# Optimization experiments

Measured on AMD Instinct MI355X. Metric: run time of the kernel, lower is better.

Reference implementation:

```python
import jax, jax.numpy as jnp
import numpy as np

B, S, WIDTH, M = 2, 240, 128, 20
PAD = 16


def setup_inputs() -> dict:
    key = jax.random.key(0)
    ks = jax.random.split(key, 10)
    scale = 1.0 / (WIDTH * WIDTH)
    inp = {
        "x": jax.random.normal(ks[0], (B, S, S, 3), jnp.float32),
        "fc0_w": jax.random.normal(ks[1], (5, WIDTH), jnp.float32) * 0.1,
        "fc0_b": jnp.zeros((WIDTH,), jnp.float32),
        # 5 spectral layers, complex weights stored as [..., 2] = (real, imag)
        "spec_w1": jax.random.uniform(ks[2], (5, WIDTH, WIDTH, M, M, 2), jnp.float32) * scale,
        "spec_w2": jax.random.uniform(ks[3], (5, WIDTH, WIDTH, M, M, 2), jnp.float32) * scale,
        # 5 residual 1x1 convs
        "w_w": jax.random.normal(ks[4], (5, WIDTH, WIDTH), jnp.float32) / np.sqrt(WIDTH),
        "w_b": jnp.zeros((5, WIDTH), jnp.float32),
        "fc1_w": jax.random.normal(ks[5], (WIDTH, WIDTH), jnp.float32) / np.sqrt(WIDTH),
        "fc1_b": jnp.zeros((WIDTH,), jnp.float32),
        # 4 heads (u, v, p, T): width->64->1
        "head1_w": jax.random.normal(ks[6], (4, WIDTH, 64), jnp.float32) / np.sqrt(WIDTH),
        "head1_b": jnp.zeros((4, 64), jnp.float32),
        "head2_w": jax.random.normal(ks[7], (4, 64, 1), jnp.float32) / 8.0,
        "head2_b": jnp.zeros((4, 1), jnp.float32),
    }
    return inp


def _spectral_conv(h, w1, w2):
    # h: (B, C, H, W) real; w1, w2: (C_in, C_out, M, M) complex64
    Hh, Ww = h.shape[-2], h.shape[-1]
    ft = jnp.fft.rfft2(h)  # (B, C, H, W//2+1)
    o1 = jnp.einsum('bixy,ioxy->boxy', ft[:, :, :M, :M], w1)
    o2 = jnp.einsum('bixy,ioxy->boxy', ft[:, :, -M:, :M], w2)
    out_ft = jnp.zeros((h.shape[0], w1.shape[1], Hh, Ww // 2 + 1), jnp.complex64)
    out_ft = out_ft.at[:, :, :M, :M].set(o1).at[:, :, -M:, :M].set(o2)
    return jnp.fft.irfft2(out_ft, s=(Hh, Ww))


def reference(x, fc0_w, fc0_b, spec_w1, spec_w2, w_w, w_b, fc1_w, fc1_b,
              head1_w, head1_b, head2_w, head2_b):
    Bn, sx, sy = x.shape[0], x.shape[1], x.shape[2]
    gx = jnp.broadcast_to(jnp.linspace(0.0, 1.0, sx, dtype=x.dtype)[None, :, None, None], (Bn, sx, sy, 1))
    gy = jnp.broadcast_to(jnp.linspace(0.0, 1.0, sy, dtype=x.dtype)[None, None, :, None], (Bn, sx, sy, 1))
    x1 = jnp.concatenate([x, gx, gy], axis=-1)          # (B, S, S, 5)
    h = x1 @ fc0_w + fc0_b                              # lift -> (B, S, S, width)
    h = jnp.transpose(h, (0, 3, 1, 2))                  # (B, width, S, S)
    h = jnp.pad(h, ((0, 0), (0, 0), (0, PAD), (0, PAD)))
    c1 = spec_w1[..., 0] + 1j * spec_w1[..., 1]
    c2 = spec_w2[..., 0] + 1j * spec_w2[..., 1]
    for i in range(5):
        s = _spectral_conv(h, c1[i], c2[i])
        lin = jnp.einsum('bchw,oc->bohw', h, w_w[i]) + w_b[i][None, :, None, None]
        h = s + lin
        if i < 4:
            h = jax.nn.gelu(h, approximate=False)
    h = h[..., :-PAD, :-PAD]
    h = jnp.transpose(h, (0, 2, 3, 1))                  # (B, S, S, width)
    h = jax.nn.gelu(h @ fc1_w + fc1_b, approximate=False)
    h1 = jax.nn.gelu(jnp.einsum('bhwc,kcd->kbhwd', h, head1_w)
                     + head1_b[:, None, None, None, :], approximate=False)
    out = jnp.einsum('kbhwd,kdo->kbhwo', h1, head2_w) + head2_b[:, None, None, None, :]
    return (out[0], out[1], out[2], out[3])  # u, v, p, T each (B, S, S, 1)
```

## Files before the change

### kernel.cpp

```cpp
#include <hip/hip_runtime.h>
#include <math.h>


#define SZ_H   (2ull*256*256*128)
#define O_HA   0ull
#define O_HB   (O_HA + SZ_H)
#define O_G    (O_HB + SZ_H)
#define SZ_G   (2ull*256*20*128*2)
#define O_FTT  (O_G + SZ_G)
#define SZ_FT  (2ull*40*20*128*2)
#define O_OFT  (O_FTT + SZ_FT)
#define O_EY   (O_OFT + SZ_FT)
#define SZ_EY  (256ull*20*2)
#define O_EX   (O_EY + SZ_EY)
#define SZ_EX  (256ull*40*2)
#define O_EXI  (O_EX + SZ_EX)
#define O_WWT  (O_EXI + SZ_EX)
#define SZ_WWT 81920ull
#define O_PART (O_WWT + SZ_WWT)
#define SZ_PART (8ull*204800*2)

static __device__ __forceinline__ float gelu_f(float v) {
    return 0.5f * v * (1.0f + erff(v * 0.70710678118654752f));
}

__global__ void k_prep(const float* __restrict__ w_w, float* __restrict__ ws) {
    int i = blockIdx.x * 256 + threadIdx.x;
    const float STEP = 6.2831853071795864769f / 256.0f;
    if (i < 5120) {
        int ky = i % 20, y = i / 20;
        int t = (ky * y) & 255;
        float th = t * STEP;
        ws[O_EY + 2*(size_t)i]     = cosf(th);
        ws[O_EY + 2*(size_t)i + 1] = -sinf(th);
    } else if (i < 15360) {
        int m = i - 5120; int j = m % 40, x = m / 40;
        int kx = (j < 20) ? j : (216 + j);
        int t = (kx * x) & 255;
        float th = t * STEP;
        ws[O_EX + 2*(size_t)m]     = cosf(th);
        ws[O_EX + 2*(size_t)m + 1] = -sinf(th);
    } else if (i < 25600) {
        int m = i - 15360; int j = m % 40, x = m / 40;
        int kx = (j < 20) ? j : (216 + j);
        int t = (kx * x) & 255;
        float th = t * STEP;
        ws[O_EXI + 2*(size_t)m]     = cosf(th);
        ws[O_EXI + 2*(size_t)m + 1] = sinf(th);
    } else {
        int m = i - 25600;
        if (m < 81920) {
            int l = m >> 14, r = m & 16383;
            int ic = r >> 7, oc = r & 127;
            ws[O_WWT + m] = w_w[(size_t)l*16384 + oc*128 + ic];
        }
    }
}

__global__ __launch_bounds__(256) void k_fc0(const float* __restrict__ xin,
        const float* __restrict__ w, const float* __restrict__ bv,
        float4* __restrict__ H4) {
    size_t e = (size_t)blockIdx.x * 256 + threadIdx.x;
    int c4 = (int)(e & 31) * 4;
    int y = (int)((e >> 5) & 255);
    int x = (int)((e >> 13) & 255);
    int b = (int)(e >> 21);
    float4 h = make_float4(0.f, 0.f, 0.f, 0.f);
    if (x < 240 && y < 240) {
        const float* xp = xin + (((size_t)(b*240 + x))*240 + y)*3;
        float x0 = xp[0], x1 = xp[1], x2 = xp[2];
        float gx = x*(1.0f/239.0f), gy = y*(1.0f/239.0f);
        float4 w0 = *(const float4*)&w[c4];
        float4 w1 = *(const float4*)&w[128 + c4];
        float4 w2 = *(const float4*)&w[256 + c4];
        float4 w3 = *(const float4*)&w[384 + c4];
        float4 w4 = *(const float4*)&w[512 + c4];
        float4 bb = *(const float4*)&bv[c4];
        h.x = bb.x + x0*w0.x + x1*w1.x + x2*w2.x + gx*w3.x + gy*w4.x;
        h.y = bb.y + x0*w0.y + x1*w1.y + x2*w2.y + gx*w3.y + gy*w4.y;
        h.z = bb.z + x0*w0.z + x1*w1.z + x2*w2.z + gx*w3.z + gy*w4.z;
        h.w = bb.w + x0*w0.w + x1*w1.w + x2*w2.w + gx*w3.w + gy*w4.w;
    }
    H4[e] = h;
}

__global__ __launch_bounds__(256) void k_ydft(const float* __restrict__ H,
        const float* __restrict__ Ey, float2* __restrict__ G) {
    int b = blockIdx.x >> 8, x = blockIdx.x & 255;
    int c = threadIdx.x & 127;
    int yq = __builtin_amdgcn_readfirstlane((int)(threadIdx.x >> 7));
    const float* Hrow = H + ((size_t)(b*256 + x)) * 256 * 128;
    float ar[20], ai[20];
    #pragma unroll
    for (int k = 0; k < 20; k++) { ar[k] = 0.f; ai[k] = 0.f; }
    for (int i = 0; i < 128; i++) {
        int y = yq*128 + i;
        float v = Hrow[(size_t)y*128 + c];
        const float* e = Ey + (size_t)y*40;
        #pragma unroll
        for (int k = 0; k < 20; k++) {
            ar[k] = fmaf(v, e[2*k],   ar[k]);
            ai[k] = fmaf(v, e[2*k+1], ai[k]);
        }
    }
    __shared__ float red[20][128][2];
    if (yq == 1) {
        #pragma unroll
        for (int k = 0; k < 20; k++) { red[k][c][0] = ar[k]; red[k][c][1] = ai[k]; }
    }
    __syncthreads();
    if (yq == 0) {
        float2* Gp = G + ((size_t)(b*256 + x))*20*128;
        #pragma unroll
        for (int k = 0; k < 20; k++)
            Gp[k*128 + c] = make_float2(ar[k] + red[k][c][0], ai[k] + red[k][c][1]);
    }
}

__global__ __launch_bounds__(256) void k_xdft(const float2* __restrict__ G,
        const float* __restrict__ Ex, float2* __restrict__ ftT) {
    int t = blockIdx.x;
    int ch = t & 3, jq = (t >> 2) & 3, ky = (t >> 4) % 20, b = t / 320;
    int cl = threadIdx.x & 31;
    int xq = threadIdx.x >> 5;
    int c = ch*32 + cl;
    int j0 = jq*10;
    float ar[10], ai[10];
    #pragma unroll
    for (int k = 0; k < 10; k++) { ar[k] = 0.f; ai[k] = 0.f; }
    for (int i = 0; i < 32; i++) {
        int x = xq*32 + i;
        float2 g = G[(((size_t)(b*256 + x))*20 + ky)*128 + c];
        const float2* e2 = (const float2*)(Ex + (size_t)x*80) + j0;
        #pragma unroll
        for (int k = 0; k < 10; k++) {
            float2 e = e2[k];
            ar[k] = fmaf(g.x, e.x, fmaf(-g.y, e.y, ar[k]));
            ai[k] = fmaf(g.x, e.y, fmaf( g.y, e.x, ai[k]));
        }
    }
    #pragma unroll
    for (int k = 0; k < 10; k++) {
        ar[k] += __shfl_xor(ar[k], 32);
        ai[k] += __shfl_xor(ai[k], 32);
    }
    __shared__ float red[3][10][32][2];
    int wid = threadIdx.x >> 6;
    int sub = threadIdx.x & 63;
    if (wid > 0 && sub < 32) {
        #pragma unroll
        for (int k = 0; k < 10; k++) { red[wid-1][k][cl][0] = ar[k]; red[wid-1][k][cl][1] = ai[k]; }
    }
    __syncthreads();
    if (wid == 0 && sub < 32) {
        #pragma unroll
        for (int k = 0; k < 10; k++) {
            float rr = ar[k], ii = ai[k];
            #pragma unroll
            for (int q = 0; q < 3; q++) { rr += red[q][k][cl][0]; ii += red[q][k][cl][1]; }
            ftT[((size_t)c*2 + b)*800 + (size_t)(j0 + k)*20 + ky] = make_float2(rr, ii);
        }
    }
}

__global__ __launch_bounds__(448) void k_modemix(const float2* __restrict__ w1,
        const float2* __restrict__ w2, const float2* __restrict__ ftT,
        float2* __restrict__ outp, int ic_per) {
    int bid = blockIdx.x & 255;
    int icq = blockIdx.x >> 8;
    int oc = bid >> 1;
    int mh = bid & 1;
    int tid = threadIdx.x;
    if (tid >= 400) return;
    int wsel = tid / 200;
    int m = mh*200 + (tid % 200);
    int jk = wsel*400 + m;
    const float2* wb = wsel ? w2 : w1;
    int ic0 = icq * ic_per;
    float ar0=0.f, ai0=0.f, ar1=0.f, ai1=0.f;
    #pragma unroll 4
    for (int i = 0; i < ic_per; i++) {
        int ic = ic0 + i;
        float2 wv = wb[((size_t)(ic*128 + oc))*400 + m];
        float2 f0 = ftT[(size_t)ic*1600 + jk];
        float2 f1 = ftT[(size_t)ic*1600 + 800 + jk];
        ar0 = fmaf(f0.x, wv.x, fmaf(-f0.y, wv.y, ar0));
        ai0 = fmaf(f0.x, wv.y, fmaf( f0.y, wv.x, ai0));
        ar1 = fmaf(f1.x, wv.x, fmaf(-f1.y, wv.y, ar1));
        ai1 = fmaf(f1.x, wv.y, fmaf( f1.y, wv.x, ai1));
    }
    float2* o = outp + (size_t)icq * 204800;
    o[(size_t)jk*128 + oc]         = make_float2(ar0, ai0);
    o[(size_t)(800 + jk)*128 + oc] = make_float2(ar1, ai1);
}

__global__ __launch_bounds__(512) void k_modered(const float2* __restrict__ part,
        float2* __restrict__ oft) {
    int i = blockIdx.x * 512 + threadIdx.x;
    if (i >= 204800) return;
    float2 s = part[i];
    #pragma unroll
    for (int q = 1; q < 8; q++) {
        float2 p = part[(size_t)q*204800 + i];
        s.x += p.x; s.y += p.y;
    }
    oft[i] = s;
}

__global__ __launch_bounds__(256) void k_xidft(const float2* __restrict__ oft,
        const float* __restrict__ Exi, float2* __restrict__ T) {
    int b = blockIdx.x >> 7, xq = blockIdx.x & 127;
    int oc = threadIdx.x & 127;
    int xs = __builtin_amdgcn_readfirstlane((int)(threadIdx.x >> 7));
    int x = xq*2 + xs;
    float ar[20], ai[20];
    #pragma unroll
    for (int k = 0; k < 20; k++) { ar[k] = 0.f; ai[k] = 0.f; }
    const float2* ob = oft + (size_t)b*800*128;
    for (int j = 0; j < 40; j++) {
        float er = Exi[(size_t)x*80 + 2*j], ei = Exi[(size_t)x*80 + 2*j + 1];
        #pragma unroll
        for (int k = 0; k < 20; k++) {
            float2 o = ob[(size_t)(j*20 + k)*128 + oc];
            ar[k] = fmaf(o.x, er, fmaf(-o.y, ei, ar[k]));
            ai[k] = fmaf(o.x, ei, fmaf( o.y, er, ai[k]));
        }
    }
    float2* Tp = T + ((size_t)(b*256 + x))*20*128;
    #pragma unroll
    for (int k = 0; k < 20; k++) Tp[k*128 + oc] = make_float2(ar[k], ai[k]);
}

__global__ __launch_bounds__(256) void k_spec_lin(const float* __restrict__ H,
        const float2* __restrict__ T, const float* __restrict__ wwT,
        const float* __restrict__ wb, float* __restrict__ Hout, int do_gelu) {
    int yg = blockIdx.x & 3;
    int x  = (blockIdx.x >> 2) & 255;
    int b  = blockIdx.x >> 10;
    int tid = threadIdx.x;
    int lane = tid & 63;
    int wv = __builtin_amdgcn_readfirstlane(tid >> 6);
    int oc0 = wv * 32;
    int y0 = yg * 64;
    __shared__ float hl[64][129];
    const float* Hbase = H + (((size_t)(b*256 + x))*256 + y0)*128;
    #pragma unroll
    for (int it = 0; it < 8; it++) {
        int i = tid + it*256;
        int pi = i >> 5, c4 = (i & 31)*4;
        float4 v = *(const float4*)&Hbase[(size_t)pi*128 + c4];
        hl[pi][c4] = v.x; hl[pi][c4+1] = v.y; hl[pi][c4+2] = v.z; hl[pi][c4+3] = v.w;
    }
    float csr[20], csi[20];
    {
        int y = y0 + lane;
        #pragma unroll
        for (int k = 0; k < 20; k++) {
            int t = (k * y) & 255;
            float th = t * (6.2831853071795864769f/256.0f);
            float f = (k == 0 ? 1.0f : 2.0f) * (1.0f/65536.0f);
            csr[k] = f * __cosf(th);
            csi[k] = f * __sinf(th);
        }
    }
    __syncthreads();
    float acc[32];
    #pragma unroll
    for (int o = 0; o < 32; o++) acc[o] = 0.f;
    for (int ic = 0; ic < 128; ic++) {
        float t = hl[lane][ic];
        const float* wr = &wwT[(size_t)ic*128 + oc0];
        #pragma unroll
        for (int o4 = 0; o4 < 8; o4++) {
            float4 w = *(const float4*)&wr[o4*4];
            acc[o4*4]   = fmaf(t, w.x, acc[o4*4]);
            acc[o4*4+1] = fmaf(t, w.y, acc[o4*4+1]);
            acc[o4*4+2] = fmaf(t, w.z, acc[o4*4+2]);
            acc[o4*4+3] = fmaf(t, w.w, acc[o4*4+3]);
        }
    }
    const float2* Tp = T + ((size_t)(b*256 + x))*20*128 + oc0;
    for (int k = 0; k < 20; k++) {
        const float2* tr = Tp + (size_t)k*128;
        float cr = csr[k], ci = csi[k];
        #pragma unroll
        for (int o = 0; o < 32; o++) {
            float2 tv = tr[o];
            acc[o] = fmaf(tv.x, cr, fmaf(-tv.y, ci, acc[o]));
        }
    }
    __syncthreads();
    const float* bp = &wb[oc0];
    #pragma unroll
    for (int o = 0; o < 32; o++) {
        float v = acc[o] + bp[o];
        if (do_gelu) v = gelu_f(v);
        hl[lane][oc0 + o] = v;
    }
    __syncthreads();
    float* Obase = Hout + (((size_t)(b*256 + x))*256 + y0)*128;
    #pragma unroll
    for (int it = 0; it < 32; it++) {
        int i = tid + it*256;
        int pi = i >> 7, c = i & 127;
        Obase[(size_t)pi*128 + c] = hl[pi][c];
    }
}

__global__ __launch_bounds__(512) void k_tail(const float* __restrict__ H,
        const float* __restrict__ fc1_w, const float* __restrict__ fc1_b,
        const float* __restrict__ h1w, const float* __restrict__ h1b,
        const float* __restrict__ h2w, const float* __restrict__ h2b,
        float* __restrict__ out) {
    int tid = threadIdx.x;
    int lane = tid & 63;
    int wv = __builtin_amdgcn_readfirstlane(tid >> 6);
    int p0 = blockIdx.x * 64;
    __shared__ float smem[8320];
    __shared__ float red[4][64];
    float (*hl)[129] = (float (*)[129])smem;
    float (*tl)[65]  = (float (*)[65])smem;
    #pragma unroll
    for (int it = 0; it < 4; it++) {
        int i = tid + it*512;
        int pi = i >> 5, c4 = (i & 31)*4;
        int p = p0 + pi;
        int bb = p / 57600, r = p % 57600;
        int xx = r / 240, yy = r % 240;
        float4 v = *(const float4*)&H[(((size_t)(bb*256 + xx))*256 + yy)*128 + c4];
        hl[pi][c4] = v.x; hl[pi][c4+1] = v.y; hl[pi][c4+2] = v.z; hl[pi][c4+3] = v.w;
    }
    __syncthreads();
    int oc0 = wv * 16;
    float acc[16];
    #pragma unroll
    for (int o = 0; o < 16; o++) acc[o] = 0.f;
    #pragma unroll 2
    for (int ic = 0; ic < 128; ic++) {
        float t = hl[lane][ic];
        const float* wr = &fc1_w[(size_t)ic*128 + oc0];
        #pragma unroll
        for (int o4 = 0; o4 < 4; o4++) {
            float4 w = *(const float4*)&wr[o4*4];
            acc[o4*4]   = fmaf(t, w.x, acc[o4*4]);
            acc[o4*4+1] = fmaf(t, w.y, acc[o4*4+1]);
            acc[o4*4+2] = fmaf(t, w.z, acc[o4*4+2]);
            acc[o4*4+3] = fmaf(t, w.w, acc[o4*4+3]);
        }
    }
    __syncthreads();
    const float* bp = &fc1_b[oc0];
    #pragma unroll
    for (int o = 0; o < 16; o++)
        tl[oc0 + o][lane] = gelu_f(acc[o] + bp[o]);
    __syncthreads();
    int k    = wv >> 1;
    int half = wv & 1;
    int d0 = half * 32;
    float a2[32];
    #pragma unroll
    for (int d = 0; d < 32; d++) a2[d] = 0.f;
    const float* wk = h1w + (size_t)k*8192 + d0;
    #pragma unroll 2
    for (int c = 0; c < 128; c++) {
        float t = tl[c][lane];
        const float* wr = &wk[c*64];
        #pragma unroll
        for (int d4 = 0; d4 < 8; d4++) {
            float4 w = *(const float4*)&wr[d4*4];
            a2[d4*4]   = fmaf(t, w.x, a2[d4*4]);
            a2[d4*4+1] = fmaf(t, w.y, a2[d4*4+1]);
            a2[d4*4+2] = fmaf(t, w.z, a2[d4*4+2]);
            a2[d4*4+3] = fmaf(t, w.w, a2[d4*4+3]);
        }
    }
    const float* b1 = &h1b[k*64 + d0];
    const float* w2 = &h2w[k*64 + d0];
    float ph = 0.f;
    #pragma unroll
    for (int d = 0; d < 32; d++)
        ph += gelu_f(a2[d] + b1[d]) * w2[d];
    if (half == 1) red[k][lane] = ph;
    __syncthreads();
    if (half == 0)
        out[(size_t)k*115200 + p0 + lane] = ph + red[k][lane] + h2b[k];
}

extern "C" void kernel_launch(void* const* d_in, const int* in_sizes, int n_in,
                              void* d_out, int out_size, void* d_ws, size_t ws_size,
                              hipStream_t stream) {
    const float* x       = (const float*)d_in[0];
    const float* fc0_w   = (const float*)d_in[1];
    const float* fc0_b   = (const float*)d_in[2];
    const float* spec_w1 = (const float*)d_in[3];
    const float* spec_w2 = (const float*)d_in[4];
    const float* w_w     = (const float*)d_in[5];
    const float* w_b     = (const float*)d_in[6];
    const float* fc1_w   = (const float*)d_in[7];
    const float* fc1_b   = (const float*)d_in[8];
    const float* head1_w = (const float*)d_in[9];
    const float* head1_b = (const float*)d_in[10];
    const float* head2_w = (const float*)d_in[11];
    const float* head2_b = (const float*)d_in[12];
    float* ws = (float*)d_ws;
    float* out = (float*)d_out;

    int split = ws_size >= (size_t)(O_PART + SZ_PART) * 4 ? 1 : 0;

    k_prep<<<420, 256, 0, stream>>>(w_w, ws);
    k_fc0<<<16384, 256, 0, stream>>>(x, fc0_w, fc0_b, (float4*)(ws + O_HA));

    float* cur = ws + O_HA;
    float* nxt = ws + O_HB;
    float2* G    = (float2*)(ws + O_G);
    float2* ftT  = (float2*)(ws + O_FTT);
    float2* oft  = (float2*)(ws + O_OFT);
    float2* part = (float2*)(ws + O_PART);

    for (int l = 0; l < 5; l++) {
        k_ydft<<<512, 256, 0, stream>>>(cur, ws + O_EY, G);
        k_xdft<<<640, 256, 0, stream>>>(G, ws + O_EX, ftT);
        const float2* w1l = (const float2*)(spec_w1 + (size_t)l*13107200);
        const float2* w2l = (const float2*)(spec_w2 + (size_t)l*13107200);
        if (split) {
            k_modemix<<<2048, 448, 0, stream>>>(w1l, w2l, ftT, part, 16);
            k_modered<<<400, 512, 0, stream>>>(part, oft);
        } else {
            k_modemix<<<256, 448, 0, stream>>>(w1l, w2l, ftT, oft, 128);
        }
        k_xidft<<<256, 256, 0, stream>>>(oft, ws + O_EXI, G);
        k_spec_lin<<<2048, 256, 0, stream>>>(cur, G, ws + O_WWT + (size_t)l*16384,
                                             w_b + l*128, nxt, (l < 4) ? 1 : 0);
        float* t = cur; cur = nxt; nxt = t;
    }
    k_tail<<<1800, 512, 0, stream>>>(cur, fc1_w, fc1_b, head1_w, head1_b,
                                     head2_w, head2_b, out);
}
```

Measured before the change: 1.875 ms.

## Split DFT kernels over mode halves and vectorize LDS access in matmul kernels

k_ydft and k_xidft now split the 20 y-modes across two blocks, giving 1024 blocks each. k_xidft also splits its j-sum across two thread halves with an LDS reduction. This adds parallelism and cuts per-thread register use. k_spec_lin and k_tail pad the LDS tiles to 132 columns and use float4 LDS reads and writes, batching 16 (or 8) input channels per load. k_modemix gets a larger unroll. The cost is that each H row is read twice in ydft, plus an extra barrier and reduction in xidft.

```diff
diff --git a/kernel.cpp b/kernel.cpp
--- a/kernel.cpp
+++ b/kernel.cpp
@@ -86,34 +86,38 @@
 
 __global__ __launch_bounds__(256) void k_ydft(const float* __restrict__ H,
         const float* __restrict__ Ey, float2* __restrict__ G) {
-    int b = blockIdx.x >> 8, x = blockIdx.x & 255;
+    int kh = blockIdx.x & 1;
+    int x  = (blockIdx.x >> 1) & 255;
+    int b  = blockIdx.x >> 9;
     int c = threadIdx.x & 127;
     int yq = __builtin_amdgcn_readfirstlane((int)(threadIdx.x >> 7));
+    int k0 = kh * 10;
     const float* Hrow = H + ((size_t)(b*256 + x)) * 256 * 128;
-    float ar[20], ai[20];
-    #pragma unroll
-    for (int k = 0; k < 20; k++) { ar[k] = 0.f; ai[k] = 0.f; }
+    float ar[10], ai[10];
+    #pragma unroll
+    for (int k = 0; k < 10; k++) { ar[k] = 0.f; ai[k] = 0.f; }
+    #pragma unroll 2
     for (int i = 0; i < 128; i++) {
         int y = yq*128 + i;
         float v = Hrow[(size_t)y*128 + c];
-        const float* e = Ey + (size_t)y*40;
-        #pragma unroll
-        for (int k = 0; k < 20; k++) {
+        const float* e = Ey + (size_t)y*40 + k0*2;
+        #pragma unroll
+        for (int k = 0; k < 10; k++) {
             ar[k] = fmaf(v, e[2*k],   ar[k]);
             ai[k] = fmaf(v, e[2*k+1], ai[k]);
         }
     }
-    __shared__ float red[20][128][2];
+    __shared__ float red[10][128][2];
     if (yq == 1) {
         #pragma unroll
-        for (int k = 0; k < 20; k++) { red[k][c][0] = ar[k]; red[k][c][1] = ai[k]; }
+        for (int k = 0; k < 10; k++) { red[k][c][0] = ar[k]; red[k][c][1] = ai[k]; }
     }
     __syncthreads();
     if (yq == 0) {
         float2* Gp = G + ((size_t)(b*256 + x))*20*128;
         #pragma unroll
-        for (int k = 0; k < 20; k++)
-            Gp[k*128 + c] = make_float2(ar[k] + red[k][c][0], ai[k] + red[k][c][1]);
+        for (int k = 0; k < 10; k++)
+            Gp[(k0 + k)*128 + c] = make_float2(ar[k] + red[k][c][0], ai[k] + red[k][c][1]);
     }
 }
 
@@ -178,7 +182,7 @@
     const float2* wb = wsel ? w2 : w1;
     int ic0 = icq * ic_per;
     float ar0=0.f, ai0=0.f, ar1=0.f, ai1=0.f;
-    #pragma unroll 4
+    #pragma unroll 8
     for (int i = 0; i < ic_per; i++) {
         int ic = ic0 + i;
         float2 wv = wb[((size_t)(ic*128 + oc))*400 + m];
@@ -209,26 +213,37 @@
 
 __global__ __launch_bounds__(256) void k_xidft(const float2* __restrict__ oft,
         const float* __restrict__ Exi, float2* __restrict__ T) {
-    int b = blockIdx.x >> 7, xq = blockIdx.x & 127;
+    int kh = blockIdx.x & 1;
+    int x  = (blockIdx.x >> 1) & 255;
+    int b  = blockIdx.x >> 9;
     int oc = threadIdx.x & 127;
-    int xs = __builtin_amdgcn_readfirstlane((int)(threadIdx.x >> 7));
-    int x = xq*2 + xs;
-    float ar[20], ai[20];
-    #pragma unroll
-    for (int k = 0; k < 20; k++) { ar[k] = 0.f; ai[k] = 0.f; }
+    int js = __builtin_amdgcn_readfirstlane((int)(threadIdx.x >> 7));
+    int k0 = kh * 10;
+    float ar[10], ai[10];
+    #pragma unroll
+    for (int k = 0; k < 10; k++) { ar[k] = 0.f; ai[k] = 0.f; }
     const float2* ob = oft + (size_t)b*800*128;
-    for (int j = 0; j < 40; j++) {
+    for (int j = js*20; j < js*20 + 20; j++) {
         float er = Exi[(size_t)x*80 + 2*j], ei = Exi[(size_t)x*80 + 2*j + 1];
         #pragma unroll
-        for (int k = 0; k < 20; k++) {
-            float2 o = ob[(size_t)(j*20 + k)*128 + oc];
+        for (int k = 0; k < 10; k++) {
+            float2 o = ob[(size_t)(j*20 + k0 + k)*128 + oc];
             ar[k] = fmaf(o.x, er, fmaf(-o.y, ei, ar[k]));
             ai[k] = fmaf(o.x, ei, fmaf( o.y, er, ai[k]));
         }
     }
-    float2* Tp = T + ((size_t)(b*256 + x))*20*128;
-    #pragma unroll
-    for (int k = 0; k < 20; k++) Tp[k*128 + oc] = make_float2(ar[k], ai[k]);
+    __shared__ float red[10][128][2];
+    if (js == 1) {
+        #pragma unroll
+        for (int k = 0; k < 10; k++) { red[k][oc][0] = ar[k]; red[k][oc][1] = ai[k]; }
+    }
+    __syncthreads();
+    if (js == 0) {
+        float2* Tp = T + ((size_t)(b*256 + x))*20*128;
+        #pragma unroll
+        for (int k = 0; k < 10; k++)
+            Tp[(k0 + k)*128 + oc] = make_float2(ar[k] + red[k][oc][0], ai[k] + red[k][oc][1]);
+    }
 }
 
 __global__ __launch_bounds__(256) void k_spec_lin(const float* __restrict__ H,
@@ -242,14 +257,37 @@
     int wv = __builtin_amdgcn_readfirstlane(tid >> 6);
     int oc0 = wv * 32;
     int y0 = yg * 64;
-    __shared__ float hl[64][129];
+    __shared__ float hl[64][132];
     const float* Hbase = H + (((size_t)(b*256 + x))*256 + y0)*128;
     #pragma unroll
     for (int it = 0; it < 8; it++) {
         int i = tid + it*256;
         int pi = i >> 5, c4 = (i & 31)*4;
         float4 v = *(const float4*)&Hbase[(size_t)pi*128 + c4];
-        hl[pi][c4] = v.x; hl[pi][c4+1] = v.y; hl[pi][c4+2] = v.z; hl[pi][c4+3] = v.w;
+        *(float4*)&hl[pi][c4] = v;
+    }
+    __syncthreads();
+    float acc[32];
+    #pragma unroll
+    for (int o = 0; o < 32; o++) acc[o] = 0.f;
+    for (int icb = 0; icb < 128; icb += 16) {
+        float tvals[16];
+        #pragma unroll
+        for (int q = 0; q < 4; q++)
+            *(float4*)&tvals[q*4] = *(const float4*)&hl[lane][icb + q*4];
+        #pragma unroll
+        for (int ii = 0; ii < 16; ii++) {
+            float t = tvals[ii];
+            const float* wr = &wwT[(size_t)(icb + ii)*128 + oc0];
+            #pragma unroll
+            for (int o4 = 0; o4 < 8; o4++) {
+                float4 w = *(const float4*)&wr[o4*4];
+                acc[o4*4]   = fmaf(t, w.x, acc[o4*4]);
+                acc[o4*4+1] = fmaf(t, w.y, acc[o4*4+1]);
+                acc[o4*4+2] = fmaf(t, w.z, acc[o4*4+2]);
+                acc[o4*4+3] = fmaf(t, w.w, acc[o4*4+3]);
+            }
+        }
     }
     float csr[20], csi[20];
     {
@@ -263,22 +301,6 @@
             csi[k] = f * __sinf(th);
         }
     }
-    __syncthreads();
-    float acc[32];
-    #pragma unroll
-    for (int o = 0; o < 32; o++) acc[o] = 0.f;
-    for (int ic = 0; ic < 128; ic++) {
-        float t = hl[lane][ic];
-        const float* wr = &wwT[(size_t)ic*128 + oc0];
-        #pragma unroll
-        for (int o4 = 0; o4 < 8; o4++) {
-            float4 w = *(const float4*)&wr[o4*4];
-            acc[o4*4]   = fmaf(t, w.x, acc[o4*4]);
-            acc[o4*4+1] = fmaf(t, w.y, acc[o4*4+1]);
-            acc[o4*4+2] = fmaf(t, w.z, acc[o4*4+2]);
-            acc[o4*4+3] = fmaf(t, w.w, acc[o4*4+3]);
-        }
-    }
     const float2* Tp = T + ((size_t)(b*256 + x))*20*128 + oc0;
     for (int k = 0; k < 20; k++) {
         const float2* tr = Tp + (size_t)k*128;
@@ -292,10 +314,14 @@
     __syncthreads();
     const float* bp = &wb[oc0];
     #pragma unroll
-    for (int o = 0; o < 32; o++) {
-        float v = acc[o] + bp[o];
-        if (do_gelu) v = gelu_f(v);
-        hl[lane][oc0 + o] = v;
+    for (int o4 = 0; o4 < 8; o4++) {
+        float4 r;
+        r.x = acc[o4*4]   + bp[o4*4];
+        r.y = acc[o4*4+1] + bp[o4*4+1];
+        r.z = acc[o4*4+2] + bp[o4*4+2];
+        r.w = acc[o4*4+3] + bp[o4*4+3];
+        if (do_gelu) { r.x = gelu_f(r.x); r.y = gelu_f(r.y); r.z = gelu_f(r.z); r.w = gelu_f(r.w); }
+        *(float4*)&hl[lane][oc0 + o4*4] = r;
     }
     __syncthreads();
     float* Obase = Hout + (((size_t)(b*256 + x))*256 + y0)*128;
@@ -316,10 +342,9 @@
     int lane = tid & 63;
     int wv = __builtin_amdgcn_readfirstlane(tid >> 6);
     int p0 = blockIdx.x * 64;
-    __shared__ float smem[8320];
+    __shared__ float smem[64*132];
     __shared__ float red[4][64];
-    float (*hl)[129] = (float (*)[129])smem;
-    float (*tl)[65]  = (float (*)[65])smem;
+    float (*hl)[132] = (float (*)[132])smem;
     #pragma unroll
     for (int it = 0; it < 4; it++) {
         int i = tid + it*512;
@@ -328,31 +353,43 @@
         int bb = p / 57600, r = p % 57600;
         int xx = r / 240, yy = r % 240;
         float4 v = *(const float4*)&H[(((size_t)(bb*256 + xx))*256 + yy)*128 + c4];
-        hl[pi][c4] = v.x; hl[pi][c4+1] = v.y; hl[pi][c4+2] = v.z; hl[pi][c4+3] = v.w;
+        *(float4*)&hl[pi][c4] = v;
     }
     __syncthreads();
     int oc0 = wv * 16;
     float acc[16];
     #pragma unroll
     for (int o = 0; o < 16; o++) acc[o] = 0.f;
-    #pragma unroll 2
-    for (int ic = 0; ic < 128; ic++) {
-        float t = hl[lane][ic];
-        const float* wr = &fc1_w[(size_t)ic*128 + oc0];
-        #pragma unroll
-        for (int o4 = 0; o4 < 4; o4++) {
-            float4 w = *(const float4*)&wr[o4*4];
-            acc[o4*4]   = fmaf(t, w.x, acc[o4*4]);
-            acc[o4*4+1] = fmaf(t, w.y, acc[o4*4+1]);
-            acc[o4*4+2] = fmaf(t, w.z, acc[o4*4+2]);
-            acc[o4*4+3] = fmaf(t, w.w, acc[o4*4+3]);
-        }
-    }
-    __syncthreads();
-    const float* bp = &fc1_b[oc0];
-    #pragma unroll
-    for (int o = 0; o < 16; o++)
-        tl[oc0 + o][lane] = gelu_f(acc[o] + bp[o]);
+    for (int icb = 0; icb < 128; icb += 16) {
+        float tvals[16];
+        #pragma unroll
+        for (int q = 0; q < 4; q++)
+            *(float4*)&tvals[q*4] = *(const float4*)&hl[lane][icb + q*4];
+        #pragma unroll
+        for (int ii = 0; ii < 16; ii++) {
+            float t = tvals[ii];
+            const float* wr = &fc1_w[(size_t)(icb + ii)*128 + oc0];
+            #pragma unroll
+            for (int o4 = 0; o4 < 4; o4++) {
+                float4 w = *(const float4*)&wr[o4*4];
+                acc[o4*4]   = fmaf(t, w.x, acc[o4*4]);
+                acc[o4*4+1] = fmaf(t, w.y, acc[o4*4+1]);
+                acc[o4*4+2] = fmaf(t, w.z, acc[o4*4+2]);
+                acc[o4*4+3] = fmaf(t, w.w, acc[o4*4+3]);
+            }
+        }
+    }
+    __syncthreads();
+    #pragma unroll
+    for (int o4 = 0; o4 < 4; o4++) {
+        float4 bb = *(const float4*)&fc1_b[oc0 + o4*4];
+        float4 r;
+        r.x = gelu_f(acc[o4*4]   + bb.x);
+        r.y = gelu_f(acc[o4*4+1] + bb.y);
+        r.z = gelu_f(acc[o4*4+2] + bb.z);
+        r.w = gelu_f(acc[o4*4+3] + bb.w);
+        *(float4*)&hl[lane][oc0 + o4*4] = r;
+    }
     __syncthreads();
     int k    = wv >> 1;
     int half = wv & 1;
@@ -361,17 +398,22 @@
     #pragma unroll
     for (int d = 0; d < 32; d++) a2[d] = 0.f;
     const float* wk = h1w + (size_t)k*8192 + d0;
-    #pragma unroll 2
-    for (int c = 0; c < 128; c++) {
-        float t = tl[c][lane];
-        const float* wr = &wk[c*64];
-        #pragma unroll
-        for (int d4 = 0; d4 < 8; d4++) {
-            float4 w = *(const float4*)&wr[d4*4];
-            a2[d4*4]   = fmaf(t, w.x, a2[d4*4]);
-            a2[d4*4+1] = fmaf(t, w.y, a2[d4*4+1]);
-            a2[d4*4+2] = fmaf(t, w.z, a2[d4*4+2]);
-            a2[d4*4+3] = fmaf(t, w.w, a2[d4*4+3]);
+    for (int cb = 0; cb < 128; cb += 8) {
+        float tvals[8];
+        *(float4*)&tvals[0] = *(const float4*)&hl[lane][cb];
+        *(float4*)&tvals[4] = *(const float4*)&hl[lane][cb + 4];
+        #pragma unroll
+        for (int cc = 0; cc < 8; cc++) {
+            float t = tvals[cc];
+            const float* wr = &wk[(cb + cc)*64];
+            #pragma unroll
+            for (int d4 = 0; d4 < 8; d4++) {
+                float4 w = *(const float4*)&wr[d4*4];
+                a2[d4*4]   = fmaf(t, w.x, a2[d4*4]);
+                a2[d4*4+1] = fmaf(t, w.y, a2[d4*4+1]);
+                a2[d4*4+2] = fmaf(t, w.z, a2[d4*4+2]);
+                a2[d4*4+3] = fmaf(t, w.w, a2[d4*4+3]);
+            }
         }
     }
     const float* b1 = &h1b[k*64 + d0];
@@ -418,7 +460,7 @@
     float2* part = (float2*)(ws + O_PART);
 
     for (int l = 0; l < 5; l++) {
-        k_ydft<<<512, 256, 0, stream>>>(cur, ws + O_EY, G);
+        k_ydft<<<1024, 256, 0, stream>>>(cur, ws + O_EY, G);
         k_xdft<<<640, 256, 0, stream>>>(G, ws + O_EX, ftT);
         const float2* w1l = (const float2*)(spec_w1 + (size_t)l*13107200);
         const float2* w2l = (const float2*)(spec_w2 + (size_t)l*13107200);
@@ -428,7 +470,7 @@
         } else {
             k_modemix<<<256, 448, 0, stream>>>(w1l, w2l, ftT, oft, 128);
         }
-        k_xidft<<<256, 256, 0, stream>>>(oft, ws + O_EXI, G);
+        k_xidft<<<1024, 256, 0, stream>>>(oft, ws + O_EXI, G);
         k_spec_lin<<<2048, 256, 0, stream>>>(cur, G, ws + O_WWT + (size_t)l*16384,
                                              w_b + l*128, nxt, (l < 4) ? 1 : 0);
         float* t = cur; cur = nxt; nxt = t;
```

Measured after the change: 1.726 ms. -7.9%, faster.
